# Kernel optimization log

Hardware: AMD Instinct MI355X
Metric: run time of the kernel (lower is better)

The kernel has to match this reference:

```python
import jax, jax.numpy as jnp
import numpy as np
from jax import lax

VOCAB, EMB, FILT, ATT, KW = 50000, 300, 400, 200, 3
B, N = 4096, 30

def setup_inputs() -> dict:
    key = jax.random.key(0)
    ks = jax.random.split(key, 7)
    encoded_title = jax.random.randint(ks[0], (B, N), 0, VOCAB)
    emb = jax.random.normal(ks[1], (VOCAB, EMB), dtype=jnp.float32) * 0.1
    conv_w = jax.random.normal(ks[2], (FILT, EMB, KW), dtype=jnp.float32) * (1.0 / np.sqrt(EMB * KW))
    conv_b = jnp.zeros((FILT,), dtype=jnp.float32)
    v = jax.random.normal(ks[3], (FILT, ATT), dtype=jnp.float32) * (1.0 / np.sqrt(FILT))
    vb = jnp.zeros((ATT,), dtype=jnp.float32)
    q = jax.random.normal(ks[4], (ATT, 1), dtype=jnp.float32) * (1.0 / np.sqrt(ATT))
    return {"encoded_title": encoded_title, "emb": emb, "conv_w": conv_w,
            "conv_b": conv_b, "v": v, "vb": vb, "q": q}

def reference(encoded_title, emb, conv_w, conv_b, v, vb, q):
    mask = (encoded_title != 0).astype(jnp.float32)          # [B, N]
    W = emb[encoded_title]                                    # [B, N, E]
    x = jnp.transpose(W, (0, 2, 1))                           # [B, E, N]
    C = lax.conv_general_dilated(x, conv_w, window_strides=(1,),
                                 padding=[(1, 1)],
                                 dimension_numbers=("NCH", "OIH", "NCH"))
    C = jnp.transpose(C, (0, 2, 1)) + conv_b                  # [B, N, F]
    C = jax.nn.relu(C)
    a = jnp.tanh(C @ v + vb)                                  # [B, N, A]
    a = (a @ q)[..., 0]                                       # [B, N]
    alpha = jax.nn.softmax(a, axis=0)                         # softmax over batch dim (faithful to dim=0)
    alpha = alpha * mask
    e = jnp.einsum("bn,bnf->bf", alpha, C)                    # batched weighted-sum pooling
    return e
```

## Files before the change

### kernel.cpp

```cpp
#include <hip/hip_runtime.h>
#include <hip/hip_bf16.h>

#define VOCAB 50000
#define EMB   300
#define FILT  400
#define ATT   200
#define BB    4096
#define NN    30

#define ATTP  208
#define KC    416

typedef short bf16x8 __attribute__((ext_vector_type(8)));
typedef float f32x4  __attribute__((ext_vector_type(4)));
typedef unsigned short u16x4 __attribute__((ext_vector_type(4)));

static __device__ __forceinline__ unsigned short f2bf(float f) {
    __hip_bfloat16 h = __float2bfloat16(f);
    union { __hip_bfloat16 h; unsigned short u; } c; c.h = h; return c.u;
}
static __device__ __forceinline__ float bf2f(unsigned short u) {
    union { unsigned int u; float f; } c; c.u = ((unsigned int)u) << 16; return c.f;
}
static __device__ __forceinline__ float fast_tanh(float x) {
    float e = __expf(2.f * x);
    return 1.f - 2.f * __builtin_amdgcn_rcpf(e + 1.f);
}

static __device__ __forceinline__ void dma16(const unsigned short* g, unsigned short* l) {
    __builtin_amdgcn_global_load_lds(
        (const __attribute__((address_space(1))) unsigned int*)(const void*)g,
        (__attribute__((address_space(3))) unsigned int*)(void*)l,
        16, 0, 0);
}

__global__ __launch_bounds__(256) void kP(const float* __restrict__ conv_w,
                                          const float* __restrict__ v,
                                          const float* __restrict__ vb,
                                          const float* __restrict__ q,
                                          unsigned short* __restrict__ Bc2,
                                          unsigned short* __restrict__ Bv2,
                                          float* __restrict__ vbp,
                                          float* __restrict__ qp) {
    int t = blockIdx.x * 256 + threadIdx.x;
    const int NBC = 750 * 512;
    if (t < NBC) {
        int tau = t >> 9, off = t & 511;
        int l = off >> 3, j = off & 7;
        int lm = l & 15, qq = l >> 4;
        int ft = tau % 25, es = (tau / 25) % 10, k = tau / 250;
        int f = ft * 16 + lm;
        int e = es * 32 + qq * 8 + j;
        float val = (e < EMB) ? conv_w[((size_t)f * EMB + e) * 3 + k] : 0.f;
        Bc2[t] = f2bf(val);
    } else {
        int t2 = t - NBC;
        if (t2 < 169 * 512) {
            int tau = t2 >> 9, off = t2 & 511;
            int l = off >> 3, j = off & 7;
            int lm = l & 15, qq = l >> 4;
            int ks = tau / 13, at = tau % 13;
            int att = at * 16 + lm;
            int fcol = ks * 32 + qq * 8 + j;
            float val = (att < ATT && fcol < FILT) ? v[(size_t)fcol * ATT + att] : 0.f;
            Bv2[t2] = f2bf(val);
        }
    }
    if (t < ATTP) {
        vbp[t] = (t < ATT) ? vb[t] : 0.f;
        qp[t]  = (t < ATT) ? q[t] : 0.f;
    }
}

static __device__ __forceinline__ void gatherA(const float* __restrict__ emb,
                                               int tok, int e, float* aR) {
#pragma unroll
    for (int jj = 0; jj < 8; jj++) aR[jj] = 0.f;
    if (tok >= 0 && e < EMB) {
        if (e <= 292) {
            float4 x = *(const float4*)(emb + (size_t)tok * EMB + e);
            float4 y = *(const float4*)(emb + (size_t)tok * EMB + e + 4);
            aR[0] = x.x; aR[1] = x.y; aR[2] = x.z; aR[3] = x.w;
            aR[4] = y.x; aR[5] = y.y; aR[6] = y.z; aR[7] = y.w;
        } else {
#pragma unroll
            for (int jj = 0; jj < 8; jj++) {
                int ee = e + jj;
                if (ee < EMB) aR[jj] = emb[(size_t)tok * EMB + ee];
            }
        }
    }
}

__global__ __launch_bounds__(640, 2) void k1_conv(
    const int* __restrict__ idx,
    const float* __restrict__ emb,
    const unsigned short* __restrict__ Bc2,
    const float* __restrict__ conv_b,
    unsigned short* __restrict__ Cws)
{
    __shared__ unsigned short As[131 * 40];
    __shared__ unsigned short Bs[2 * 25 * 512];
    const int bid = blockIdx.x;
    const int t = threadIdx.x;
    const int lane = t & 63, wave = t >> 6;
    const int lm = lane & 15, qq = lane >> 4;
    const int wg = wave / 5, fw = wave % 5;
    const int rbase = wg * 64;

    const int uj = t >> 2, useg = t & 3;
    const bool uact = (t < 524);
    int utok = -1;
    if (uact && uj < 128) {
        int ub = uj >> 5, uj2 = uj & 31;
        if (uj2 >= 1 && uj2 <= 30) utok = idx[(bid * 4 + ub) * NN + (uj2 - 1)];
    }

    if (wg == 0) {
#pragma unroll
        for (int s = 0; s < 2; s++) {
#pragma unroll
            for (int nt = 0; nt < 5; nt++) {
                int gt = (s % 3) * 250 + (s / 3) * 25 + fw * 5 + nt;
                dma16(Bc2 + (size_t)gt * 512 + lane * 8,
                      Bs + s * 12800 + (fw * 5 + nt) * 512);
            }
        }
    }
    float aR[8];
    gatherA(emb, utok, useg * 8, aR);

    f32x4 acc[4][5];
#pragma unroll
    for (int mt = 0; mt < 4; mt++)
#pragma unroll
        for (int nt = 0; nt < 5; nt++)
            acc[mt][nt] = (f32x4){0.f, 0.f, 0.f, 0.f};

    for (int es = 0; es < 10; ++es) {
        if (uact) {
            union { bf16x8 v; unsigned short u[8]; } cv;
#pragma unroll
            for (int jj = 0; jj < 8; jj++) cv.u[jj] = f2bf(aR[jj]);
            *(bf16x8*)(As + uj * 40 + useg * 8) = cv.v;
        }
        __syncthreads();
        if (es < 9) gatherA(emb, utok, (es + 1) * 32 + useg * 8, aR);

#pragma unroll
        for (int k = 0; k < 3; ++k) {
            const int s = es * 3 + k;
            const unsigned short* bb = Bs + (s & 1) * 12800;
            bf16x8 aF[4];
#pragma unroll
            for (int mt = 0; mt < 4; mt++)
                aF[mt] = *(const bf16x8*)(As + (rbase + mt * 16 + lm + k) * 40 + qq * 8);
#pragma unroll
            for (int nt = 0; nt < 5; nt++) {
                bf16x8 bF = *(const bf16x8*)(bb + (fw * 5 + nt) * 512 + lane * 8);
#pragma unroll
                for (int mt = 0; mt < 4; mt++)
                    acc[mt][nt] = __builtin_amdgcn_mfma_f32_16x16x32_bf16(aF[mt], bF, acc[mt][nt], 0, 0, 0);
            }
            __syncthreads();
            if (s + 2 < 30 && wg == 0) {
                const int s2 = s + 2, es2 = s2 / 3, k2 = s2 - es2 * 3;
#pragma unroll
                for (int nt = 0; nt < 5; nt++) {
                    int gt = (k2 * 10 + es2) * 25 + fw * 5 + nt;
                    dma16(Bc2 + (size_t)gt * 512 + lane * 8,
                          Bs + (s & 1) * 12800 + (fw * 5 + nt) * 512);
                }
            }
        }
    }

    const int f0 = fw * 80;
    float cb[5];
#pragma unroll
    for (int nt = 0; nt < 5; nt++) cb[nt] = conv_b[f0 + nt * 16 + lm];
#pragma unroll
    for (int mt = 0; mt < 4; mt++) {
#pragma unroll
        for (int r = 0; r < 4; r++) {
            int lrow = rbase + mt * 16 + qq * 4 + r;
            int n = lrow & 31;
            int bglob = bid * 4 + (lrow >> 5);
            if (n < NN) {
#pragma unroll
                for (int nt = 0; nt < 5; nt++) {
                    float vv = fmaxf(acc[mt][nt][r] + cb[nt], 0.f);
                    Cws[((size_t)bglob * NN + n) * FILT + f0 + nt * 16 + lm] = f2bf(vv);
                }
            }
        }
    }
}

__global__ __launch_bounds__(256, 2) void k2_att(
    const unsigned short* __restrict__ Cws,
    const unsigned short* __restrict__ Bv2,
    const float* __restrict__ vbp, const float* __restrict__ qp,
    float* __restrict__ a_out)
{
    __shared__ unsigned short Bs[2 * 13 * 512];
    const int lane = threadIdx.x & 63;
    const int wave = threadIdx.x >> 6;
    const int lm = lane & 15, qq = lane >> 4;
    const int r0 = blockIdx.x * 128 + wave * 32;

#pragma unroll
    for (int s = 0; s < 2; s++)
#pragma unroll
        for (int nt = 0; nt < 13; nt++)
            if ((nt & 3) == wave)
                dma16(Bv2 + (size_t)(s * 13 + nt) * 512 + lane * 8,
                      Bs + s * 6656 + nt * 512);

    bf16x8 aFc[2], aFn[2];
#pragma unroll
    for (int mt = 0; mt < 2; mt++)
        aFc[mt] = *(const bf16x8*)(Cws + (size_t)(r0 + mt * 16 + lm) * FILT + 8 * qq);

    f32x4 acc[2][13];
#pragma unroll
    for (int mt = 0; mt < 2; mt++)
#pragma unroll
        for (int nt = 0; nt < 13; nt++) acc[mt][nt] = (f32x4){0.f, 0.f, 0.f, 0.f};

    __syncthreads();

    for (int ks = 0; ks < 13; ++ks) {
        if (ks < 12)
#pragma unroll
            for (int mt = 0; mt < 2; mt++)
                aFn[mt] = *(const bf16x8*)(Cws + (size_t)(r0 + mt * 16 + lm) * FILT + (ks + 1) * 32 + 8 * qq);
        const unsigned short* bb = Bs + (ks & 1) * 6656;
#pragma unroll
        for (int nt = 0; nt < 13; nt++) {
            bf16x8 bF = *(const bf16x8*)(bb + nt * 512 + lane * 8);
#pragma unroll
            for (int mt = 0; mt < 2; mt++)
                acc[mt][nt] = __builtin_amdgcn_mfma_f32_16x16x32_bf16(aFc[mt], bF, acc[mt][nt], 0, 0, 0);
        }
        __syncthreads();
        if (ks + 2 < 13)
#pragma unroll
            for (int nt = 0; nt < 13; nt++)
                if ((nt & 3) == wave)
                    dma16(Bv2 + (size_t)((ks + 2) * 13 + nt) * 512 + lane * 8,
                          Bs + (ks & 1) * 6656 + nt * 512);
#pragma unroll
        for (int mt = 0; mt < 2; mt++) aFc[mt] = aFn[mt];
    }

#pragma unroll
    for (int mt = 0; mt < 2; mt++) {
        float rs[4] = {0.f, 0.f, 0.f, 0.f};
#pragma unroll
        for (int nt = 0; nt < 13; nt++) {
            int att = nt * 16 + lm;
            float vbv = vbp[att], qv = qp[att];
#pragma unroll
            for (int r = 0; r < 4; r++)
                rs[r] += fast_tanh(acc[mt][nt][r] + vbv) * qv;
        }
#pragma unroll
        for (int off = 1; off < 16; off <<= 1)
#pragma unroll
            for (int r = 0; r < 4; r++) rs[r] += __shfl_xor(rs[r], off, 64);
        if (lm == 0) {
#pragma unroll
            for (int r = 0; r < 4; r++) {
                int rg = r0 + mt * 16 + qq * 4 + r;
                a_out[(size_t)(rg % NN) * BB + (rg / NN)] = rs[r];
            }
        }
    }
}

__global__ __launch_bounds__(1024) void k3_softmax(float* __restrict__ a,
                                                   const int* __restrict__ idx) {
    int n = blockIdx.x, tid = threadIdx.x;
    float4 v4 = *(const float4*)(a + (size_t)n * BB + tid * 4);
    float m = fmaxf(fmaxf(v4.x, v4.y), fmaxf(v4.z, v4.w));
    __shared__ float red[32];
#pragma unroll
    for (int off = 32; off >= 1; off >>= 1) m = fmaxf(m, __shfl_xor(m, off, 64));
    int wv = tid >> 6;
    if ((tid & 63) == 0) red[wv] = m;
    __syncthreads();
#pragma unroll
    for (int w = 0; w < 16; w++) m = fmaxf(m, red[w]);
    float e0 = expf(v4.x - m), e1 = expf(v4.y - m);
    float e2 = expf(v4.z - m), e3 = expf(v4.w - m);
    float s = e0 + e1 + e2 + e3;
#pragma unroll
    for (int off = 32; off >= 1; off >>= 1) s += __shfl_xor(s, off, 64);
    if ((tid & 63) == 0) red[16 + wv] = s;
    __syncthreads();
    s = 0.f;
#pragma unroll
    for (int w = 0; w < 16; w++) s += red[16 + w];
    float inv = 1.f / s;
    int b0 = tid * 4;
    float4 o;
    o.x = e0 * inv * ((idx[(size_t)(b0 + 0) * NN + n] != 0) ? 1.f : 0.f);
    o.y = e1 * inv * ((idx[(size_t)(b0 + 1) * NN + n] != 0) ? 1.f : 0.f);
    o.z = e2 * inv * ((idx[(size_t)(b0 + 2) * NN + n] != 0) ? 1.f : 0.f);
    o.w = e3 * inv * ((idx[(size_t)(b0 + 3) * NN + n] != 0) ? 1.f : 0.f);
    *(float4*)(a + (size_t)n * BB + b0) = o;
}

__global__ __launch_bounds__(128) void k4_pool(
    const float* __restrict__ alpha, const unsigned short* __restrict__ C,
    float* __restrict__ out)
{
    int b = blockIdx.x;
    int tid = threadIdx.x;
    __shared__ float al[NN];
    if (tid < NN) al[tid] = alpha[(size_t)tid * BB + b];
    __syncthreads();
    if (tid < 100) {
        int f = tid * 4;
        float s0 = 0.f, s1 = 0.f, s2 = 0.f, s3 = 0.f;
        const unsigned short* Cb = C + (size_t)b * (NN * FILT) + f;
#pragma unroll
        for (int n = 0; n < NN; n++) {
            u16x4 c = *(const u16x4*)(Cb + (size_t)n * FILT);
            float a = al[n];
            s0 = fmaf(a, bf2f(c[0]), s0);
            s1 = fmaf(a, bf2f(c[1]), s1);
            s2 = fmaf(a, bf2f(c[2]), s2);
            s3 = fmaf(a, bf2f(c[3]), s3);
        }
        float4 o; o.x = s0; o.y = s1; o.z = s2; o.w = s3;
        *(float4*)(out + (size_t)b * FILT + f) = o;
    }
}

extern "C" void kernel_launch(void* const* d_in, const int* in_sizes, int n_in,
                              void* d_out, int out_size, void* d_ws, size_t ws_size,
                              hipStream_t stream) {
    const int*   idx    = (const int*)d_in[0];
    const float* emb    = (const float*)d_in[1];
    const float* conv_w = (const float*)d_in[2];
    const float* conv_b = (const float*)d_in[3];
    const float* v      = (const float*)d_in[4];
    const float* vb     = (const float*)d_in[5];
    const float* q      = (const float*)d_in[6];
    float* out = (float*)d_out;

    char* ws = (char*)d_ws;
    size_t o = 0;
    unsigned short* Bv2 = (unsigned short*)(ws + o); o += (size_t)169 * 512 * 2;
    float* vbp = (float*)(ws + o);                   o += 1024;
    float* qp  = (float*)(ws + o);                   o += 1024;
    unsigned short* Bc2 = (unsigned short*)(ws + o);
    float* a_buf = (float*)(ws + o);
    o += (size_t)750 * 512 * 2;
    unsigned short* Cws = (unsigned short*)(ws + o);

    const int NP = 750 * 512 + 169 * 512;
    kP<<<(NP + 255) / 256, 256, 0, stream>>>(conv_w, v, vb, q, Bc2, Bv2, vbp, qp);
    k1_conv<<<BB / 4, 640, 0, stream>>>(idx, emb, Bc2, conv_b, Cws);
    k2_att<<<(BB * NN) / 128, 256, 0, stream>>>(Cws, Bv2, vbp, qp, a_buf);
    k3_softmax<<<NN, 1024, 0, stream>>>(a_buf, idx);
    k4_pool<<<BB, 128, 0, stream>>>(a_buf, Cws, out);
}
```

Measured before the change: 276.1 us.

## Split conv waves into DMA stagers and gatherers with explicit waitcnt barriers

In the conv kernel, waves 0-4 now issue the weight DMA into LDS, and waves 5-9 gather embedding rows with 16-float loads per thread. __syncthreads is replaced by raw s_barrier with hand-placed vmcnt and lgkmcnt waits, so outstanding global loads no longer drain at every barrier. Launch bounds occupancy hints rise from 2 to 3 for both the conv and attention kernels. This adds a barrier per k-step, and the higher occupancy target may force register spills.

Measured after the change: 269.4 us, median of 2. -2.4%, faster.

```diff
diff --git a/kernel.cpp b/kernel.cpp
--- a/kernel.cpp
+++ b/kernel.cpp
@@ -32,6 +32,18 @@
         (const __attribute__((address_space(1))) unsigned int*)(const void*)g,
         (__attribute__((address_space(3))) unsigned int*)(void*)l,
         16, 0, 0);
+}
+
+#define CFENCE() asm volatile("" ::: "memory")
+static __device__ __forceinline__ void bar_lgkm0() {
+    asm volatile("s_waitcnt lgkmcnt(0)" ::: "memory");
+    __builtin_amdgcn_s_barrier();
+    CFENCE();
+}
+static __device__ __forceinline__ void bar_plain() {
+    CFENCE();
+    __builtin_amdgcn_s_barrier();
+    CFENCE();
 }
 
 __global__ __launch_bounds__(256) void kP(const float* __restrict__ conv_w,
@@ -72,27 +84,19 @@
     }
 }
 
-static __device__ __forceinline__ void gatherA(const float* __restrict__ emb,
-                                               int tok, int e, float* aR) {
-#pragma unroll
-    for (int jj = 0; jj < 8; jj++) aR[jj] = 0.f;
-    if (tok >= 0 && e < EMB) {
-        if (e <= 292) {
-            float4 x = *(const float4*)(emb + (size_t)tok * EMB + e);
-            float4 y = *(const float4*)(emb + (size_t)tok * EMB + e + 4);
-            aR[0] = x.x; aR[1] = x.y; aR[2] = x.z; aR[3] = x.w;
-            aR[4] = y.x; aR[5] = y.y; aR[6] = y.z; aR[7] = y.w;
-        } else {
-#pragma unroll
-            for (int jj = 0; jj < 8; jj++) {
-                int ee = e + jj;
-                if (ee < EMB) aR[jj] = emb[(size_t)tok * EMB + ee];
-            }
-        }
-    }
-}
-
-__global__ __launch_bounds__(640, 2) void k1_conv(
+static __device__ __forceinline__ void gather16(const float* __restrict__ emb,
+                                                int tok, int e0, float4* aR4) {
+#pragma unroll
+    for (int c = 0; c < 4; c++) {
+        float4 z; z.x = 0.f; z.y = 0.f; z.z = 0.f; z.w = 0.f;
+        int ee = e0 + c * 4;
+        if (tok >= 0 && ee < EMB)
+            z = *(const float4*)(emb + (size_t)tok * EMB + ee);
+        aR4[c] = z;
+    }
+}
+
+__global__ __launch_bounds__(640, 3) void k1_conv(
     const int* __restrict__ idx,
     const float* __restrict__ emb,
     const unsigned short* __restrict__ Bc2,
@@ -107,28 +111,32 @@
     const int lm = lane & 15, qq = lane >> 4;
     const int wg = wave / 5, fw = wave % 5;
     const int rbase = wg * 64;
-
-    const int uj = t >> 2, useg = t & 3;
-    const bool uact = (t < 524);
+    const bool stager = (wave < 5);
+
+    const int g = t - 320;
+    const int uj = g >> 1, uh = g & 1;
+    const bool gact = (!stager) && (g < 262);
     int utok = -1;
-    if (uact && uj < 128) {
+    if (gact && uj < 128) {
         int ub = uj >> 5, uj2 = uj & 31;
         if (uj2 >= 1 && uj2 <= 30) utok = idx[(bid * 4 + ub) * NN + (uj2 - 1)];
     }
 
-    if (wg == 0) {
+    float4 aR4[4];
+    if (stager) {
 #pragma unroll
         for (int s = 0; s < 2; s++) {
 #pragma unroll
             for (int nt = 0; nt < 5; nt++) {
-                int gt = (s % 3) * 250 + (s / 3) * 25 + fw * 5 + nt;
+                int gt = s * 250 + fw * 5 + nt;
                 dma16(Bc2 + (size_t)gt * 512 + lane * 8,
                       Bs + s * 12800 + (fw * 5 + nt) * 512);
             }
         }
-    }
-    float aR[8];
-    gatherA(emb, utok, useg * 8, aR);
+        asm volatile("s_waitcnt vmcnt(5)" ::: "memory");
+    } else if (gact) {
+        gather16(emb, utok, uh * 16, aR4);
+    }
 
     f32x4 acc[4][5];
 #pragma unroll
@@ -138,14 +146,17 @@
             acc[mt][nt] = (f32x4){0.f, 0.f, 0.f, 0.f};
 
     for (int es = 0; es < 10; ++es) {
-        if (uact) {
-            union { bf16x8 v; unsigned short u[8]; } cv;
-#pragma unroll
-            for (int jj = 0; jj < 8; jj++) cv.u[jj] = f2bf(aR[jj]);
-            *(bf16x8*)(As + uj * 40 + useg * 8) = cv.v;
-        }
-        __syncthreads();
-        if (es < 9) gatherA(emb, utok, (es + 1) * 32 + useg * 8, aR);
+        if (gact) {
+            const float* af = (const float*)aR4;
+            union { bf16x8 v; unsigned short u[8]; } cv0, cv1;
+#pragma unroll
+            for (int jj = 0; jj < 8; jj++) { cv0.u[jj] = f2bf(af[jj]); cv1.u[jj] = f2bf(af[8 + jj]); }
+            *(bf16x8*)(As + uj * 40 + uh * 16) = cv0.v;
+            *(bf16x8*)(As + uj * 40 + uh * 16 + 8) = cv1.v;
+        }
+        bar_lgkm0();
+        if (gact && es < 9)
+            gather16(emb, utok, (es + 1) * 32 + uh * 16, aR4);
 
 #pragma unroll
         for (int k = 0; k < 3; ++k) {
@@ -162,16 +173,22 @@
                 for (int mt = 0; mt < 4; mt++)
                     acc[mt][nt] = __builtin_amdgcn_mfma_f32_16x16x32_bf16(aF[mt], bF, acc[mt][nt], 0, 0, 0);
             }
-            __syncthreads();
-            if (s + 2 < 30 && wg == 0) {
-                const int s2 = s + 2, es2 = s2 / 3, k2 = s2 - es2 * 3;
-#pragma unroll
-                for (int nt = 0; nt < 5; nt++) {
-                    int gt = (k2 * 10 + es2) * 25 + fw * 5 + nt;
-                    dma16(Bc2 + (size_t)gt * 512 + lane * 8,
-                          Bs + (s & 1) * 12800 + (fw * 5 + nt) * 512);
+            bar_lgkm0();
+            if (stager) {
+                if (k == 0 || es < 9) {
+                    const int s2 = s + 2, es2 = s2 / 3, k2 = s2 - es2 * 3;
+#pragma unroll
+                    for (int nt = 0; nt < 5; nt++) {
+                        int gt = (k2 * 10 + es2) * 25 + fw * 5 + nt;
+                        dma16(Bc2 + (size_t)gt * 512 + lane * 8,
+                              Bs + (s & 1) * 12800 + (fw * 5 + nt) * 512);
+                    }
+                    asm volatile("s_waitcnt vmcnt(5)" ::: "memory");
+                } else {
+                    asm volatile("s_waitcnt vmcnt(0)" ::: "memory");
                 }
             }
+            bar_plain();
         }
     }
 
@@ -197,7 +214,7 @@
     }
 }
 
-__global__ __launch_bounds__(256, 2) void k2_att(
+__global__ __launch_bounds__(256, 3) void k2_att(
     const unsigned short* __restrict__ Cws,
     const unsigned short* __restrict__ Bv2,
     const float* __restrict__ vbp, const float* __restrict__ qp,
```
